# Optimization experiments

Measured on AMD Instinct MI355X. Metric: run time of the kernel, lower is better.

Reference implementation:

```python
import jax, jax.numpy as jnp
import numpy as np

B = 2
N_PER = 100000
M_PER = 27648
C = 32
Z, Y, X = 21, 400, 352
MAX_RANGE = (2, 2, 2)
RADIUS = 8.0
NSAMPLE = 16
VS = np.array([0.2, 0.2, 0.4], np.float32)  # voxel size (x, y, z)


def setup_inputs() -> dict:
    key = jax.random.key(0)
    ks = jax.random.split(key, 6)
    N = B * N_PER
    M = B * M_PER
    space = jnp.array([X * VS[0], Y * VS[1], Z * VS[2]], jnp.float32)
    xyz = jax.random.uniform(ks[0], (N, 3), jnp.float32) * space
    zc = jax.random.randint(ks[1], (M,), 0, Z)
    yc = jax.random.randint(ks[2], (M,), 0, Y)
    xc = jax.random.randint(ks[3], (M,), 0, X)
    bq = jnp.repeat(jnp.arange(B, dtype=jnp.int32), M_PER)
    new_coords = jnp.stack([bq, zc, yc, xc], 1).astype(jnp.int32)
    new_xyz = jnp.stack([(xc + 0.5) * VS[0], (yc + 0.5) * VS[1], (zc + 0.5) * VS[2]], 1).astype(jnp.float32)
    features = jax.random.normal(ks[4], (N, C), jnp.float32)
    raw = jax.random.randint(ks[5], (B, Z, Y, X), -N_PER, N_PER)
    offs = (jnp.arange(B) * N_PER)[:, None, None, None]
    voxel2point_indices = jnp.where(raw < 0, -1, raw + offs).astype(jnp.int32)
    xyz_batch_cnt = jnp.full((B,), N_PER, jnp.int32)
    new_xyz_batch_cnt = jnp.full((B,), M_PER, jnp.int32)
    return dict(new_coords=new_coords, xyz=xyz, xyz_batch_cnt=xyz_batch_cnt,
                new_xyz=new_xyz, new_xyz_batch_cnt=new_xyz_batch_cnt,
                features=features, voxel2point_indices=voxel2point_indices)


def _voxel_query(xyz, new_xyz, new_coords, point_indices):
    """Vectorized equivalent of the CUDA voxel_query kernel.
    Returns (idx (M, nsample) int32 global point indices, empty_ball_mask (M,) bool)."""
    zr, yr, xr = MAX_RANGE
    _, Zg, Yg, Xg = point_indices.shape
    M = new_coords.shape[0]
    dz, dy, dx = jnp.meshgrid(jnp.arange(-zr, zr + 1), jnp.arange(-yr, yr + 1),
                              jnp.arange(-xr, xr + 1), indexing='ij')
    offs = jnp.stack([dz.ravel(), dy.ravel(), dx.ravel()], 1)  # (K,3) in CUDA loop order z,y,x
    nb = new_coords[:, None, 1:4] + offs[None]                 # (M,K,3) candidate voxels
    lim = jnp.array([Zg, Yg, Xg])
    inb = jnp.all((nb >= 0) & (nb < lim), -1)                  # (M,K) in-bounds
    nbc = jnp.clip(nb, 0, lim - 1)
    b = new_coords[:, 0]
    pidx = point_indices[b[:, None], nbc[..., 0], nbc[..., 1], nbc[..., 2]]  # (M,K)
    valid = inb & (pidx >= 0)
    pts = xyz[jnp.maximum(pidx, 0)]                            # (M,K,3)
    d2 = jnp.sum((pts - new_xyz[:, None, :]) ** 2, -1)
    valid = valid & (d2 < RADIUS * RADIUS)
    cnt = jnp.minimum(valid.sum(-1), NSAMPLE)                  # (M,)
    # assign each valid candidate its in-order slot; overflow/invalid go to dump column
    slot = jnp.cumsum(valid, -1) - 1
    slot = jnp.where(valid & (slot < NSAMPLE), slot, NSAMPLE)
    rows = jnp.arange(M)[:, None]
    idx = jnp.zeros((M, NSAMPLE + 1), jnp.int32).at[rows, slot].set(pidx)[:, :NSAMPLE]
    first = idx[:, 0]  # CUDA pre-fills all slots with first found index
    idx = jnp.where(jnp.arange(NSAMPLE)[None, :] < cnt[:, None], idx, first[:, None])
    empty = cnt == 0
    idx = jnp.where(empty[:, None], 0, idx)
    return idx, empty


def reference(new_coords, xyz, xyz_batch_cnt, new_xyz, new_xyz_batch_cnt, features, voxel2point_indices):
    idx, empty = _voxel_query(xyz, new_xyz, new_coords, voxel2point_indices)
    # global -> batch-relative (as in the torch loop), empty balls -> 0 of their batch
    xyz_offs = jnp.concatenate([jnp.zeros(1, jnp.int32), jnp.cumsum(xyz_batch_cnt)[:-1].astype(jnp.int32)])
    qb = new_coords[:, 0]
    idx_rel = jnp.where(empty[:, None], 0, idx - xyz_offs[qb][:, None])
    # grouping_operation (stack version): gather with batch offset added back
    gidx = idx_rel + xyz_offs[qb][:, None]                     # (M, nsample) global indices
    grouped_xyz = jnp.transpose(xyz[gidx], (0, 2, 1))          # (M, 3, nsample)
    grouped_features = jnp.transpose(features[gidx], (0, 2, 1))  # (M, C, nsample)
    return grouped_features, grouped_xyz, empty
```

## Files before the change

kernel.cpp:

```cpp
#include <hip/hip_runtime.h>


constexpr int ZG = 21;
constexpr int YG = 400;
constexpr int XG = 352;
constexpr int NS = 16;
constexpr int CF = 32;
constexpr float R2 = 64.0f;

__global__ __launch_bounds__(256) void vqg_kernel(
    const int*   __restrict__ new_coords,
    const float* __restrict__ xyz,
    const int*   __restrict__ xyz_batch_cnt,
    const float* __restrict__ new_xyz,
    const float* __restrict__ features,
    const int*   __restrict__ v2p,
    float* __restrict__ out_feat,
    float* __restrict__ out_xyz,
    float* __restrict__ out_empty,
    int M)
{
    const int lane = threadIdx.x & 63;
    const int wid  = threadIdx.x >> 6;
    const int m    = blockIdx.x * 4 + wid;
    __shared__ int sg[4][NS];

    const bool active = (m < M);
    int cnt  = 0;
    int boff = 0;

    if (active) {
        const int4 qc = *reinterpret_cast<const int4*>(new_coords + (size_t)m * 4);
        const int b = qc.x, zc = qc.y, yc = qc.z, xc = qc.w;
        const float qx = new_xyz[m * 3 + 0];
        const float qy = new_xyz[m * 3 + 1];
        const float qz = new_xyz[m * 3 + 2];
        for (int i = 0; i < b; ++i) boff += xyz_batch_cnt[i];
        const int* __restrict__ gb = v2p + (size_t)b * (ZG * YG * XG);

        #pragma unroll
        for (int pass = 0; pass < 2; ++pass) {
            const int n = pass * 64 + lane;
            int  pidx  = -1;
            bool valid = false;
            if (n < 125) {
                const int dz = n / 25 - 2;
                const int dy = (n / 5) % 5 - 2;
                const int dx = n % 5 - 2;
                const int z = zc + dz, y = yc + dy, x = xc + dx;
                if ((unsigned)z < (unsigned)ZG && (unsigned)y < (unsigned)YG &&
                    (unsigned)x < (unsigned)XG) {
                    pidx = gb[((size_t)z * YG + y) * XG + x];
                    if (pidx >= 0) {
                        const float ddx = xyz[(size_t)pidx * 3 + 0] - qx;
                        const float ddy = xyz[(size_t)pidx * 3 + 1] - qy;
                        const float ddz = xyz[(size_t)pidx * 3 + 2] - qz;
                        const float d2 = __fadd_rn(
                            __fadd_rn(__fmul_rn(ddx, ddx), __fmul_rn(ddy, ddy)),
                            __fmul_rn(ddz, ddz));
                        valid = d2 < R2;
                    }
                }
            }
            const unsigned long long bal = __ballot(valid);
            const int pos = cnt + (int)__popcll(bal & ((1ull << lane) - 1ull));
            if (valid && pos < NS) sg[wid][pos] = pidx;
            cnt += (int)__popcll(bal);
            if (cnt >= NS) break;
        }
    }
    __syncthreads();

    if (active && lane < NS) {
        int g;
        if (cnt == 0) {
            g = boff;
        } else {
            const int first = sg[wid][0];
            const int c = cnt < NS ? cnt : NS;
            g = (lane < c) ? sg[wid][lane] : first;
        }
        sg[wid][lane] = g;
    }
    __syncthreads();

    if (active) {
        if (lane < 48) {
            const int s = lane & 15;
            const int d = lane >> 4;
            out_xyz[(size_t)m * 48 + d * 16 + s] =
                xyz[(size_t)sg[wid][s] * 3 + d];
        }
        if (lane == 0) out_empty[m] = (cnt == 0) ? 1.0f : 0.0f;

        float* __restrict__ of = out_feat + (size_t)m * (CF * NS);
        #pragma unroll
        for (int k = 0; k < 2; ++k) {
            const int f0 = k * 256 + lane * 4;
            const int c  = f0 >> 4;
            const int s0 = f0 & 15;
            float4 v;
            v.x = features[(size_t)sg[wid][s0 + 0] * CF + c];
            v.y = features[(size_t)sg[wid][s0 + 1] * CF + c];
            v.z = features[(size_t)sg[wid][s0 + 2] * CF + c];
            v.w = features[(size_t)sg[wid][s0 + 3] * CF + c];
            *reinterpret_cast<float4*>(of + f0) = v;
        }
    }
}

extern "C" void kernel_launch(void* const* d_in, const int* in_sizes, int n_in,
                              void* d_out, int out_size, void* d_ws, size_t ws_size,
                              hipStream_t stream) {
    const int*   new_coords    = (const int*)d_in[0];
    const float* xyz           = (const float*)d_in[1];
    const int*   xyz_batch_cnt = (const int*)d_in[2];
    const float* new_xyz       = (const float*)d_in[3];
    const float* features      = (const float*)d_in[5];
    const int*   v2p           = (const int*)d_in[6];

    const int M = in_sizes[0] / 4;

    float* out_feat  = (float*)d_out;
    float* out_xyz   = out_feat + (size_t)M * CF * NS;
    float* out_empty = out_xyz + (size_t)M * 3 * NS;

    const int blocks = (M + 3) / 4;
    vqg_kernel<<<blocks, 256, 0, stream>>>(
        new_coords, xyz, xyz_batch_cnt, new_xyz, features, v2p,
        out_feat, out_xyz, out_empty, M);
}
```

Baseline: 60.09 us.

## Stage features in LDS, pad xyz to float4, issue both neighbor passes together

Adds a prepass kernel that pads xyz into a float4 workspace copy, so each point load is a single 16-byte read. Both 64-lane neighbor passes now issue their voxel and point loads together instead of looping with an early break. Feature rows for the selected samples are read coalesced into a shared-memory tile, then transposed out with nontemporal float4 stores. In exchange it adds a second launch and a full pass over xyz, more shared memory per block, and an extra barrier. Early termination after 16 hits is gone.

```diff
diff --git a/kernel.cpp b/kernel.cpp
--- a/kernel.cpp
+++ b/kernel.cpp
@@ -8,13 +8,27 @@
 constexpr int CF = 32;
 constexpr float R2 = 64.0f;
 
+typedef float v4f __attribute__((ext_vector_type(4)));
+
+__global__ __launch_bounds__(256) void pad_xyz_kernel(
+    const float* __restrict__ xyz, float4* __restrict__ xyz4, int N)
+{
+    const int i = blockIdx.x * 256 + threadIdx.x;
+    if (i < N) {
+        const float* p = xyz + (size_t)i * 3;
+        xyz4[i] = make_float4(p[0], p[1], p[2], 0.0f);
+    }
+}
+
+template<bool USE4>
 __global__ __launch_bounds__(256) void vqg_kernel(
-    const int*   __restrict__ new_coords,
-    const float* __restrict__ xyz,
-    const int*   __restrict__ xyz_batch_cnt,
-    const float* __restrict__ new_xyz,
-    const float* __restrict__ features,
-    const int*   __restrict__ v2p,
+    const int*    __restrict__ new_coords,
+    const float*  __restrict__ xyz,
+    const float4* __restrict__ xyz4,
+    const int*    __restrict__ xyz_batch_cnt,
+    const float*  __restrict__ new_xyz,
+    const float*  __restrict__ features,
+    const int*    __restrict__ v2p,
     float* __restrict__ out_feat,
     float* __restrict__ out_xyz,
     float* __restrict__ out_empty,
@@ -23,7 +37,8 @@
     const int lane = threadIdx.x & 63;
     const int wid  = threadIdx.x >> 6;
     const int m    = blockIdx.x * 4 + wid;
-    __shared__ int sg[4][NS];
+    __shared__ int   sg[4][NS];
+    __shared__ float tile[4][NS][33];
 
     const bool active = (m < M);
     int cnt  = 0;
@@ -38,36 +53,71 @@
         for (int i = 0; i < b; ++i) boff += xyz_batch_cnt[i];
         const int* __restrict__ gb = v2p + (size_t)b * (ZG * YG * XG);
 
-        #pragma unroll
-        for (int pass = 0; pass < 2; ++pass) {
-            const int n = pass * 64 + lane;
-            int  pidx  = -1;
-            bool valid = false;
-            if (n < 125) {
-                const int dz = n / 25 - 2;
-                const int dy = (n / 5) % 5 - 2;
-                const int dx = n % 5 - 2;
-                const int z = zc + dz, y = yc + dy, x = xc + dx;
-                if ((unsigned)z < (unsigned)ZG && (unsigned)y < (unsigned)YG &&
-                    (unsigned)x < (unsigned)XG) {
-                    pidx = gb[((size_t)z * YG + y) * XG + x];
-                    if (pidx >= 0) {
-                        const float ddx = xyz[(size_t)pidx * 3 + 0] - qx;
-                        const float ddy = xyz[(size_t)pidx * 3 + 1] - qy;
-                        const float ddz = xyz[(size_t)pidx * 3 + 2] - qz;
-                        const float d2 = __fadd_rn(
-                            __fadd_rn(__fmul_rn(ddx, ddx), __fmul_rn(ddy, ddy)),
-                            __fmul_rn(ddz, ddz));
-                        valid = d2 < R2;
-                    }
-                }
+        const int n0 = lane;
+        const int n1 = 64 + lane;
+        int pidx0 = -1, pidx1 = -1;
+        {
+            const int z = zc + (n0 / 25 - 2);
+            const int y = yc + ((n0 / 5) % 5 - 2);
+            const int x = xc + (n0 % 5 - 2);
+            if ((unsigned)z < (unsigned)ZG && (unsigned)y < (unsigned)YG &&
+                (unsigned)x < (unsigned)XG)
+                pidx0 = gb[((size_t)z * YG + y) * XG + x];
+        }
+        if (n1 < 125) {
+            const int z = zc + (n1 / 25 - 2);
+            const int y = yc + ((n1 / 5) % 5 - 2);
+            const int x = xc + (n1 % 5 - 2);
+            if ((unsigned)z < (unsigned)ZG && (unsigned)y < (unsigned)YG &&
+                (unsigned)x < (unsigned)XG)
+                pidx1 = gb[((size_t)z * YG + y) * XG + x];
+        }
+
+        float p0x = 0, p0y = 0, p0z = 0, p1x = 0, p1y = 0, p1z = 0;
+        if (pidx0 >= 0) {
+            if (USE4) {
+                const float4 p = xyz4[pidx0];
+                p0x = p.x; p0y = p.y; p0z = p.z;
+            } else {
+                p0x = xyz[(size_t)pidx0 * 3 + 0];
+                p0y = xyz[(size_t)pidx0 * 3 + 1];
+                p0z = xyz[(size_t)pidx0 * 3 + 2];
             }
-            const unsigned long long bal = __ballot(valid);
-            const int pos = cnt + (int)__popcll(bal & ((1ull << lane) - 1ull));
-            if (valid && pos < NS) sg[wid][pos] = pidx;
-            cnt += (int)__popcll(bal);
-            if (cnt >= NS) break;
-        }
+        }
+        if (pidx1 >= 0) {
+            if (USE4) {
+                const float4 p = xyz4[pidx1];
+                p1x = p.x; p1y = p.y; p1z = p.z;
+            } else {
+                p1x = xyz[(size_t)pidx1 * 3 + 0];
+                p1y = xyz[(size_t)pidx1 * 3 + 1];
+                p1z = xyz[(size_t)pidx1 * 3 + 2];
+            }
+        }
+
+        bool v0 = false, v1 = false;
+        if (pidx0 >= 0) {
+            const float dx = p0x - qx, dy = p0y - qy, dz = p0z - qz;
+            const float d2 = __fadd_rn(__fadd_rn(__fmul_rn(dx, dx), __fmul_rn(dy, dy)),
+                                       __fmul_rn(dz, dz));
+            v0 = d2 < R2;
+        }
+        if (pidx1 >= 0) {
+            const float dx = p1x - qx, dy = p1y - qy, dz = p1z - qz;
+            const float d2 = __fadd_rn(__fadd_rn(__fmul_rn(dx, dx), __fmul_rn(dy, dy)),
+                                       __fmul_rn(dz, dz));
+            v1 = d2 < R2;
+        }
+
+        const unsigned long long below = (1ull << lane) - 1ull;
+        const unsigned long long bal0 = __ballot(v0);
+        const unsigned long long bal1 = __ballot(v1);
+        const int c0   = (int)__popcll(bal0);
+        const int pos0 = (int)__popcll(bal0 & below);
+        const int pos1 = c0 + (int)__popcll(bal1 & below);
+        if (v0 && pos0 < NS) sg[wid][pos0] = pidx0;
+        if (v1 && pos1 < NS) sg[wid][pos1] = pidx1;
+        cnt = c0 + (int)__popcll(bal1);
     }
     __syncthreads();
 
@@ -76,11 +126,20 @@
         if (cnt == 0) {
             g = boff;
         } else {
-            const int first = sg[wid][0];
             const int c = cnt < NS ? cnt : NS;
-            g = (lane < c) ? sg[wid][lane] : first;
+            g = (lane < c) ? sg[wid][lane] : sg[wid][0];
         }
         sg[wid][lane] = g;
+    }
+    __syncthreads();
+
+    const int K = active ? (cnt > 0 ? (cnt < NS ? cnt : NS) : 1) : 0;
+    if (active) {
+        const int half = lane >> 5;
+        const int c    = lane & 31;
+        for (int r = half; r < K; r += 2) {
+            tile[wid][r][c] = features[(size_t)sg[wid][r] * CF + c];
+        }
     }
     __syncthreads();
 
@@ -88,23 +147,27 @@
         if (lane < 48) {
             const int s = lane & 15;
             const int d = lane >> 4;
-            out_xyz[(size_t)m * 48 + d * 16 + s] =
-                xyz[(size_t)sg[wid][s] * 3 + d];
-        }
-        if (lane == 0) out_empty[m] = (cnt == 0) ? 1.0f : 0.0f;
+            const int row = sg[wid][s];
+            const float val = USE4 ? reinterpret_cast<const float*>(xyz4 + row)[d]
+                                   : xyz[(size_t)row * 3 + d];
+            __builtin_nontemporal_store(val, out_xyz + (size_t)m * 48 + d * 16 + s);
+        }
+        if (lane == 0)
+            __builtin_nontemporal_store(cnt == 0 ? 1.0f : 0.0f, out_empty + m);
 
         float* __restrict__ of = out_feat + (size_t)m * (CF * NS);
         #pragma unroll
         for (int k = 0; k < 2; ++k) {
-            const int f0 = k * 256 + lane * 4;
-            const int c  = f0 >> 4;
-            const int s0 = f0 & 15;
-            float4 v;
-            v.x = features[(size_t)sg[wid][s0 + 0] * CF + c];
-            v.y = features[(size_t)sg[wid][s0 + 1] * CF + c];
-            v.z = features[(size_t)sg[wid][s0 + 2] * CF + c];
-            v.w = features[(size_t)sg[wid][s0 + 3] * CF + c];
-            *reinterpret_cast<float4*>(of + f0) = v;
+            const int c  = k * 16 + (lane >> 2);
+            const int s0 = (lane & 3) * 4;
+            v4f v;
+            #pragma unroll
+            for (int j = 0; j < 4; ++j) {
+                const int s = s0 + j;
+                v[j] = tile[wid][s < K ? s : 0][c];
+            }
+            __builtin_nontemporal_store(
+                v, reinterpret_cast<v4f*>(of + k * 256 + (lane << 2)));
         }
     }
 }
@@ -120,13 +183,24 @@
     const int*   v2p           = (const int*)d_in[6];
 
     const int M = in_sizes[0] / 4;
+    const int N = in_sizes[1] / 3;
 
     float* out_feat  = (float*)d_out;
     float* out_xyz   = out_feat + (size_t)M * CF * NS;
     float* out_empty = out_xyz + (size_t)M * 3 * NS;
 
     const int blocks = (M + 3) / 4;
-    vqg_kernel<<<blocks, 256, 0, stream>>>(
-        new_coords, xyz, xyz_batch_cnt, new_xyz, features, v2p,
-        out_feat, out_xyz, out_empty, M);
+    const bool use4 = ws_size >= (size_t)N * sizeof(float4);
+
+    if (use4) {
+        float4* xyz4 = (float4*)d_ws;
+        pad_xyz_kernel<<<(N + 255) / 256, 256, 0, stream>>>(xyz, xyz4, N);
+        vqg_kernel<true><<<blocks, 256, 0, stream>>>(
+            new_coords, xyz, xyz4, xyz_batch_cnt, new_xyz, features, v2p,
+            out_feat, out_xyz, out_empty, M);
+    } else {
+        vqg_kernel<false><<<blocks, 256, 0, stream>>>(
+            new_coords, xyz, nullptr, xyz_batch_cnt, new_xyz, features, v2p,
+            out_feat, out_xyz, out_empty, M);
+    }
 }
```

Result: slower. 61.85 us (+2.9%).

## Process two queries per wavefront with register permutes instead of shared memory

Applied to the files above, without the earlier changes.

Each wavefront now handles two queries and issues all four voxel-grid lookups and their xyz loads up front, so the memory requests overlap instead of running in dependent passes. Compaction of valid neighbour indices moves from shared memory with __syncthreads to ds_permute and shuffles, and the outputs are written with nontemporal stores. It also drops the early exit once 16 neighbours are found, so the second-pass loads are always issued, and it raises register pressure.

```diff
diff --git a/kernel.cpp b/kernel.cpp
--- a/kernel.cpp
+++ b/kernel.cpp
@@ -7,6 +7,14 @@
 constexpr int NS = 16;
 constexpr int CF = 32;
 constexpr float R2 = 64.0f;
+
+typedef float v4f __attribute__((ext_vector_type(4)));
+
+struct QState {
+    int  cnt;
+    int  boff;
+    int  gfin;
+};
 
 __global__ __launch_bounds__(256) void vqg_kernel(
     const int*   __restrict__ new_coords,
@@ -21,90 +29,170 @@
     int M)
 {
     const int lane = threadIdx.x & 63;
-    const int wid  = threadIdx.x >> 6;
-    const int m    = blockIdx.x * 4 + wid;
-    __shared__ int sg[4][NS];
-
-    const bool active = (m < M);
-    int cnt  = 0;
-    int boff = 0;
-
-    if (active) {
-        const int4 qc = *reinterpret_cast<const int4*>(new_coords + (size_t)m * 4);
-        const int b = qc.x, zc = qc.y, yc = qc.z, xc = qc.w;
-        const float qx = new_xyz[m * 3 + 0];
-        const float qy = new_xyz[m * 3 + 1];
-        const float qz = new_xyz[m * 3 + 2];
-        for (int i = 0; i < b; ++i) boff += xyz_batch_cnt[i];
-        const int* __restrict__ gb = v2p + (size_t)b * (ZG * YG * XG);
-
-        #pragma unroll
-        for (int pass = 0; pass < 2; ++pass) {
-            const int n = pass * 64 + lane;
-            int  pidx  = -1;
-            bool valid = false;
-            if (n < 125) {
-                const int dz = n / 25 - 2;
-                const int dy = (n / 5) % 5 - 2;
-                const int dx = n % 5 - 2;
-                const int z = zc + dz, y = yc + dy, x = xc + dx;
-                if ((unsigned)z < (unsigned)ZG && (unsigned)y < (unsigned)YG &&
-                    (unsigned)x < (unsigned)XG) {
-                    pidx = gb[((size_t)z * YG + y) * XG + x];
-                    if (pidx >= 0) {
-                        const float ddx = xyz[(size_t)pidx * 3 + 0] - qx;
-                        const float ddy = xyz[(size_t)pidx * 3 + 1] - qy;
-                        const float ddz = xyz[(size_t)pidx * 3 + 2] - qz;
-                        const float d2 = __fadd_rn(
-                            __fadd_rn(__fmul_rn(ddx, ddx), __fmul_rn(ddy, ddy)),
-                            __fmul_rn(ddz, ddz));
-                        valid = d2 < R2;
-                    }
-                }
+    const int w    = (blockIdx.x * 256 + threadIdx.x) >> 6;
+    const int m0   = w * 2;
+    const int m1   = m0 + 1;
+    if (m0 >= M) return;
+    const bool has1 = (m1 < M);
+
+    const int4 qc0 = *reinterpret_cast<const int4*>(new_coords + (size_t)m0 * 4);
+    const int4 qc1 = has1 ? *reinterpret_cast<const int4*>(new_coords + (size_t)m1 * 4) : qc0;
+    const float qx0 = new_xyz[m0 * 3 + 0], qy0 = new_xyz[m0 * 3 + 1], qz0 = new_xyz[m0 * 3 + 2];
+    const float qx1 = has1 ? new_xyz[m1 * 3 + 0] : 0.f;
+    const float qy1 = has1 ? new_xyz[m1 * 3 + 1] : 0.f;
+    const float qz1 = has1 ? new_xyz[m1 * 3 + 2] : 0.f;
+
+    int boff0 = 0, boff1 = 0;
+    for (int i = 0; i < qc0.x; ++i) boff0 += xyz_batch_cnt[i];
+    for (int i = 0; i < qc1.x; ++i) boff1 += xyz_batch_cnt[i];
+
+    const int n0 = lane;
+    const int n1 = 64 + lane;
+    const int dz0 = n0 / 25 - 2, dy0 = (n0 / 5) % 5 - 2, dx0 = n0 % 5 - 2;
+    const int dz1 = n1 / 25 - 2, dy1 = (n1 / 5) % 5 - 2, dx1 = n1 % 5 - 2;
+    const bool in1 = (n1 < 125);
+
+    const int* __restrict__ gb0 = v2p + (size_t)qc0.x * (ZG * YG * XG);
+    const int* __restrict__ gb1 = v2p + (size_t)qc1.x * (ZG * YG * XG);
+
+    int pa0 = -1, pa1 = -1, pb0 = -1, pb1 = -1;
+    {
+        const int z = qc0.y + dz0, y = qc0.z + dy0, x = qc0.w + dx0;
+        if ((unsigned)z < (unsigned)ZG && (unsigned)y < (unsigned)YG && (unsigned)x < (unsigned)XG)
+            pa0 = gb0[((size_t)z * YG + y) * XG + x];
+    }
+    {
+        const int z = qc0.y + dz1, y = qc0.z + dy1, x = qc0.w + dx1;
+        if (in1 && (unsigned)z < (unsigned)ZG && (unsigned)y < (unsigned)YG && (unsigned)x < (unsigned)XG)
+            pa1 = gb0[((size_t)z * YG + y) * XG + x];
+    }
+    if (has1) {
+        const int z = qc1.y + dz0, y = qc1.z + dy0, x = qc1.w + dx0;
+        if ((unsigned)z < (unsigned)ZG && (unsigned)y < (unsigned)YG && (unsigned)x < (unsigned)XG)
+            pb0 = gb1[((size_t)z * YG + y) * XG + x];
+    }
+    if (has1) {
+        const int z = qc1.y + dz1, y = qc1.z + dy1, x = qc1.w + dx1;
+        if (in1 && (unsigned)z < (unsigned)ZG && (unsigned)y < (unsigned)YG && (unsigned)x < (unsigned)XG)
+            pb1 = gb1[((size_t)z * YG + y) * XG + x];
+    }
+
+    float a0x = 0, a0y = 0, a0z = 0, a1x = 0, a1y = 0, a1z = 0;
+    float b0x = 0, b0y = 0, b0z = 0, b1x = 0, b1y = 0, b1z = 0;
+    if (pa0 >= 0) { const float* p = xyz + (size_t)pa0 * 3; a0x = p[0]; a0y = p[1]; a0z = p[2]; }
+    if (pa1 >= 0) { const float* p = xyz + (size_t)pa1 * 3; a1x = p[0]; a1y = p[1]; a1z = p[2]; }
+    if (pb0 >= 0) { const float* p = xyz + (size_t)pb0 * 3; b0x = p[0]; b0y = p[1]; b0z = p[2]; }
+    if (pb1 >= 0) { const float* p = xyz + (size_t)pb1 * 3; b1x = p[0]; b1y = p[1]; b1z = p[2]; }
+
+    bool va0 = false, va1 = false, vb0 = false, vb1 = false;
+    if (pa0 >= 0) {
+        const float dx = a0x - qx0, dy = a0y - qy0, dz = a0z - qz0;
+        va0 = __fadd_rn(__fadd_rn(__fmul_rn(dx, dx), __fmul_rn(dy, dy)), __fmul_rn(dz, dz)) < R2;
+    }
+    if (pa1 >= 0) {
+        const float dx = a1x - qx0, dy = a1y - qy0, dz = a1z - qz0;
+        va1 = __fadd_rn(__fadd_rn(__fmul_rn(dx, dx), __fmul_rn(dy, dy)), __fmul_rn(dz, dz)) < R2;
+    }
+    if (pb0 >= 0) {
+        const float dx = b0x - qx1, dy = b0y - qy1, dz = b0z - qz1;
+        vb0 = __fadd_rn(__fadd_rn(__fmul_rn(dx, dx), __fmul_rn(dy, dy)), __fmul_rn(dz, dz)) < R2;
+    }
+    if (pb1 >= 0) {
+        const float dx = b1x - qx1, dy = b1y - qy1, dz = b1z - qz1;
+        vb1 = __fadd_rn(__fadd_rn(__fmul_rn(dx, dx), __fmul_rn(dy, dy)), __fmul_rn(dz, dz)) < R2;
+    }
+
+    const unsigned long long below = (1ull << lane) - 1ull;
+    const int junk = (16 + (lane & 31)) << 2;
+
+    int cnt0, gfin0;
+    {
+        const unsigned long long bal0 = __ballot(va0);
+        const unsigned long long bal1 = __ballot(va1);
+        const int c0   = (int)__popcll(bal0);
+        cnt0 = c0 + (int)__popcll(bal1);
+        const int pos0 = (int)__popcll(bal0 & below);
+        const int pos1 = c0 + (int)__popcll(bal1 & below);
+        const int addr0 = (va0 && pos0 < NS) ? (pos0 << 2) : junk;
+        const int addr1 = (va1 && pos1 < NS) ? (pos1 << 2) : junk;
+        const int perm0 = __builtin_amdgcn_ds_permute(addr0, pa0);
+        const int perm1 = __builtin_amdgcn_ds_permute(addr1, pa1);
+        const int sel   = (lane < c0) ? perm0 : perm1;
+        const int first = __shfl(sel, 0);
+        const int c16   = cnt0 < NS ? cnt0 : NS;
+        gfin0 = (cnt0 == 0) ? boff0 : (((lane & 15) < c16) ? sel : first);
+    }
+    int cnt1 = 0, gfin1 = 0;
+    if (has1) {
+        const unsigned long long bal0 = __ballot(vb0);
+        const unsigned long long bal1 = __ballot(vb1);
+        const int c0   = (int)__popcll(bal0);
+        cnt1 = c0 + (int)__popcll(bal1);
+        const int pos0 = (int)__popcll(bal0 & below);
+        const int pos1 = c0 + (int)__popcll(bal1 & below);
+        const int addr0 = (vb0 && pos0 < NS) ? (pos0 << 2) : junk;
+        const int addr1 = (vb1 && pos1 < NS) ? (pos1 << 2) : junk;
+        const int perm0 = __builtin_amdgcn_ds_permute(addr0, pb0);
+        const int perm1 = __builtin_amdgcn_ds_permute(addr1, pb1);
+        const int sel   = (lane < c0) ? perm0 : perm1;
+        const int first = __shfl(sel, 0);
+        const int c16   = cnt1 < NS ? cnt1 : NS;
+        gfin1 = (cnt1 == 0) ? boff1 : (((lane & 15) < c16) ? sel : first);
+    }
+
+    const int s0lane = (lane & 3) << 2;
+    const int a_r0 = __shfl(gfin0, s0lane + 0);
+    const int a_r1 = __shfl(gfin0, s0lane + 1);
+    const int a_r2 = __shfl(gfin0, s0lane + 2);
+    const int a_r3 = __shfl(gfin0, s0lane + 3);
+    const int b_r0 = __shfl(gfin1, s0lane + 0);
+    const int b_r1 = __shfl(gfin1, s0lane + 1);
+    const int b_r2 = __shfl(gfin1, s0lane + 2);
+    const int b_r3 = __shfl(gfin1, s0lane + 3);
+
+    {
+        const int s = lane & 15;
+        const int d = lane >> 4;
+        if (lane < 48) {
+            const int row = __shfl(gfin0, s);
+            __builtin_nontemporal_store(xyz[(size_t)row * 3 + d],
+                                        out_xyz + (size_t)m0 * 48 + d * 16 + s);
+        }
+        if (lane == 0)
+            __builtin_nontemporal_store(cnt0 == 0 ? 1.0f : 0.0f, out_empty + m0);
+        if (has1) {
+            if (lane < 48) {
+                const int row = __shfl(gfin1, s);
+                __builtin_nontemporal_store(xyz[(size_t)row * 3 + d],
+                                            out_xyz + (size_t)m1 * 48 + d * 16 + s);
             }
-            const unsigned long long bal = __ballot(valid);
-            const int pos = cnt + (int)__popcll(bal & ((1ull << lane) - 1ull));
-            if (valid && pos < NS) sg[wid][pos] = pidx;
-            cnt += (int)__popcll(bal);
-            if (cnt >= NS) break;
+            if (lane == 0)
+                __builtin_nontemporal_store(cnt1 == 0 ? 1.0f : 0.0f, out_empty + m1);
         }
     }
-    __syncthreads();
-
-    if (active && lane < NS) {
-        int g;
-        if (cnt == 0) {
-            g = boff;
-        } else {
-            const int first = sg[wid][0];
-            const int c = cnt < NS ? cnt : NS;
-            g = (lane < c) ? sg[wid][lane] : first;
-        }
-        sg[wid][lane] = g;
-    }
-    __syncthreads();
-
-    if (active) {
-        if (lane < 48) {
-            const int s = lane & 15;
-            const int d = lane >> 4;
-            out_xyz[(size_t)m * 48 + d * 16 + s] =
-                xyz[(size_t)sg[wid][s] * 3 + d];
-        }
-        if (lane == 0) out_empty[m] = (cnt == 0) ? 1.0f : 0.0f;
-
-        float* __restrict__ of = out_feat + (size_t)m * (CF * NS);
+
+    float* __restrict__ of0 = out_feat + (size_t)m0 * (CF * NS);
+    float* __restrict__ of1 = out_feat + (size_t)m1 * (CF * NS);
+    #pragma unroll
+    for (int k = 0; k < 2; ++k) {
+        const int c = k * 16 + (lane >> 2);
+        v4f v;
+        v[0] = features[(size_t)a_r0 * CF + c];
+        v[1] = features[(size_t)a_r1 * CF + c];
+        v[2] = features[(size_t)a_r2 * CF + c];
+        v[3] = features[(size_t)a_r3 * CF + c];
+        __builtin_nontemporal_store(v, reinterpret_cast<v4f*>(of0 + k * 256 + (lane << 2)));
+    }
+    if (has1) {
         #pragma unroll
         for (int k = 0; k < 2; ++k) {
-            const int f0 = k * 256 + lane * 4;
-            const int c  = f0 >> 4;
-            const int s0 = f0 & 15;
-            float4 v;
-            v.x = features[(size_t)sg[wid][s0 + 0] * CF + c];
-            v.y = features[(size_t)sg[wid][s0 + 1] * CF + c];
-            v.z = features[(size_t)sg[wid][s0 + 2] * CF + c];
-            v.w = features[(size_t)sg[wid][s0 + 3] * CF + c];
-            *reinterpret_cast<float4*>(of + f0) = v;
+            const int c = k * 16 + (lane >> 2);
+            v4f v;
+            v[0] = features[(size_t)b_r0 * CF + c];
+            v[1] = features[(size_t)b_r1 * CF + c];
+            v[2] = features[(size_t)b_r2 * CF + c];
+            v[3] = features[(size_t)b_r3 * CF + c];
+            __builtin_nontemporal_store(v, reinterpret_cast<v4f*>(of1 + k * 256 + (lane << 2)));
         }
     }
 }
@@ -125,7 +213,8 @@
     float* out_xyz   = out_feat + (size_t)M * CF * NS;
     float* out_empty = out_xyz + (size_t)M * 3 * NS;
 
-    const int blocks = (M + 3) / 4;
+    const int waves  = (M + 1) / 2;
+    const int blocks = (waves + 3) / 4;
     vqg_kernel<<<blocks, 256, 0, stream>>>(
         new_coords, xyz, xyz_batch_cnt, new_xyz, features, v2p,
         out_feat, out_xyz, out_empty, M);
```

Result: faster. 53.43 us (-11.1%).

## Process four queries per wavefront with register-only compaction and batched loads

Applied to the files above, without the earlier changes.

Each wavefront now handles four queries instead of one. All grid lookups, point-coordinate loads and feature gathers for those queries are issued up front to increase memory-level parallelism. Shared memory and __syncthreads are replaced by ballot plus ds_permute compaction and shuffles, and outputs use nontemporal stores. In exchange there are four times fewer wavefronts, higher register pressure, and the early exit once sixteen neighbours are found is gone, so the second pass is always loaded.

```diff
diff --git a/kernel.cpp b/kernel.cpp
--- a/kernel.cpp
+++ b/kernel.cpp
@@ -7,6 +7,9 @@
 constexpr int NS = 16;
 constexpr int CF = 32;
 constexpr float R2 = 64.0f;
+constexpr int QPW = 4;
+
+typedef float v4f __attribute__((ext_vector_type(4)));
 
 __global__ __launch_bounds__(256) void vqg_kernel(
     const int*   __restrict__ new_coords,
@@ -21,90 +24,153 @@
     int M)
 {
     const int lane = threadIdx.x & 63;
-    const int wid  = threadIdx.x >> 6;
-    const int m    = blockIdx.x * 4 + wid;
-    __shared__ int sg[4][NS];
+    const int w    = (blockIdx.x * 256 + threadIdx.x) >> 6;
+    const int mb   = w * QPW;
+    if (mb >= M) return;
 
-    const bool active = (m < M);
-    int cnt  = 0;
-    int boff = 0;
+    bool has[QPW];
+    #pragma unroll
+    for (int q = 0; q < QPW; ++q) has[q] = (mb + q) < M;
 
-    if (active) {
-        const int4 qc = *reinterpret_cast<const int4*>(new_coords + (size_t)m * 4);
-        const int b = qc.x, zc = qc.y, yc = qc.z, xc = qc.w;
-        const float qx = new_xyz[m * 3 + 0];
-        const float qy = new_xyz[m * 3 + 1];
-        const float qz = new_xyz[m * 3 + 2];
-        for (int i = 0; i < b; ++i) boff += xyz_batch_cnt[i];
-        const int* __restrict__ gb = v2p + (size_t)b * (ZG * YG * XG);
+    int4  qc[QPW];
+    float qx[QPW], qy[QPW], qz[QPW];
+    int   boff[QPW];
+    #pragma unroll
+    for (int q = 0; q < QPW; ++q) {
+        const int m = has[q] ? (mb + q) : mb;
+        qc[q] = *reinterpret_cast<const int4*>(new_coords + (size_t)m * 4);
+        qx[q] = new_xyz[m * 3 + 0];
+        qy[q] = new_xyz[m * 3 + 1];
+        qz[q] = new_xyz[m * 3 + 2];
+        int bo = 0;
+        for (int i = 0; i < qc[q].x; ++i) bo += xyz_batch_cnt[i];
+        boff[q] = bo;
+    }
 
-        #pragma unroll
-        for (int pass = 0; pass < 2; ++pass) {
-            const int n = pass * 64 + lane;
-            int  pidx  = -1;
-            bool valid = false;
-            if (n < 125) {
-                const int dz = n / 25 - 2;
-                const int dy = (n / 5) % 5 - 2;
-                const int dx = n % 5 - 2;
-                const int z = zc + dz, y = yc + dy, x = xc + dx;
-                if ((unsigned)z < (unsigned)ZG && (unsigned)y < (unsigned)YG &&
-                    (unsigned)x < (unsigned)XG) {
-                    pidx = gb[((size_t)z * YG + y) * XG + x];
-                    if (pidx >= 0) {
-                        const float ddx = xyz[(size_t)pidx * 3 + 0] - qx;
-                        const float ddy = xyz[(size_t)pidx * 3 + 1] - qy;
-                        const float ddz = xyz[(size_t)pidx * 3 + 2] - qz;
-                        const float d2 = __fadd_rn(
-                            __fadd_rn(__fmul_rn(ddx, ddx), __fmul_rn(ddy, ddy)),
-                            __fmul_rn(ddz, ddz));
-                        valid = d2 < R2;
-                    }
-                }
-            }
-            const unsigned long long bal = __ballot(valid);
-            const int pos = cnt + (int)__popcll(bal & ((1ull << lane) - 1ull));
-            if (valid && pos < NS) sg[wid][pos] = pidx;
-            cnt += (int)__popcll(bal);
-            if (cnt >= NS) break;
+    const int n1 = 64 + lane;
+    const int dz0 = lane / 25 - 2, dy0 = (lane / 5) % 5 - 2, dx0 = lane % 5 - 2;
+    const int dz1 = n1 / 25 - 2,   dy1 = (n1 / 5) % 5 - 2,   dx1 = n1 % 5 - 2;
+    const bool in1 = (n1 < 125);
+
+    int pidx[QPW][2];
+    #pragma unroll
+    for (int q = 0; q < QPW; ++q) {
+        const int* __restrict__ gb = v2p + (size_t)qc[q].x * (ZG * YG * XG);
+        pidx[q][0] = -1;
+        pidx[q][1] = -1;
+        {
+            const int z = qc[q].y + dz0, y = qc[q].z + dy0, x = qc[q].w + dx0;
+            if ((unsigned)z < (unsigned)ZG && (unsigned)y < (unsigned)YG &&
+                (unsigned)x < (unsigned)XG)
+                pidx[q][0] = gb[((size_t)z * YG + y) * XG + x];
+        }
+        {
+            const int z = qc[q].y + dz1, y = qc[q].z + dy1, x = qc[q].w + dx1;
+            if (in1 && (unsigned)z < (unsigned)ZG && (unsigned)y < (unsigned)YG &&
+                (unsigned)x < (unsigned)XG)
+                pidx[q][1] = gb[((size_t)z * YG + y) * XG + x];
         }
     }
-    __syncthreads();
 
-    if (active && lane < NS) {
-        int g;
-        if (cnt == 0) {
-            g = boff;
-        } else {
-            const int first = sg[wid][0];
-            const int c = cnt < NS ? cnt : NS;
-            g = (lane < c) ? sg[wid][lane] : first;
+    float px[QPW][2], py[QPW][2], pz[QPW][2];
+    #pragma unroll
+    for (int q = 0; q < QPW; ++q) {
+        #pragma unroll
+        for (int p = 0; p < 2; ++p) {
+            px[q][p] = 0.f; py[q][p] = 0.f; pz[q][p] = 0.f;
+            if (pidx[q][p] >= 0) {
+                const float* r = xyz + (size_t)pidx[q][p] * 3;
+                px[q][p] = r[0]; py[q][p] = r[1]; pz[q][p] = r[2];
+            }
         }
-        sg[wid][lane] = g;
     }
-    __syncthreads();
 
-    if (active) {
-        if (lane < 48) {
-            const int s = lane & 15;
-            const int d = lane >> 4;
-            out_xyz[(size_t)m * 48 + d * 16 + s] =
-                xyz[(size_t)sg[wid][s] * 3 + d];
+    bool val[QPW][2];
+    #pragma unroll
+    for (int q = 0; q < QPW; ++q) {
+        #pragma unroll
+        for (int p = 0; p < 2; ++p) {
+            bool v = false;
+            if (pidx[q][p] >= 0) {
+                const float dx = px[q][p] - qx[q];
+                const float dy = py[q][p] - qy[q];
+                const float dz = pz[q][p] - qz[q];
+                v = __fadd_rn(__fadd_rn(__fmul_rn(dx, dx), __fmul_rn(dy, dy)),
+                              __fmul_rn(dz, dz)) < R2;
+            }
+            val[q][p] = v;
         }
-        if (lane == 0) out_empty[m] = (cnt == 0) ? 1.0f : 0.0f;
+    }
 
-        float* __restrict__ of = out_feat + (size_t)m * (CF * NS);
+    const unsigned long long below = (1ull << lane) - 1ull;
+    const int junk = (16 + (lane & 31)) << 2;
+
+    int cnt[QPW], gfin[QPW];
+    #pragma unroll
+    for (int q = 0; q < QPW; ++q) {
+        const unsigned long long bal0 = __ballot(val[q][0]);
+        const unsigned long long bal1 = __ballot(val[q][1]);
+        const int c0   = (int)__popcll(bal0);
+        cnt[q] = c0 + (int)__popcll(bal1);
+        const int pos0 = (int)__popcll(bal0 & below);
+        const int pos1 = c0 + (int)__popcll(bal1 & below);
+        const int addr0 = (val[q][0] && pos0 < NS) ? (pos0 << 2) : junk;
+        const int addr1 = (val[q][1] && pos1 < NS) ? (pos1 << 2) : junk;
+        const int perm0 = __builtin_amdgcn_ds_permute(addr0, pidx[q][0]);
+        const int perm1 = __builtin_amdgcn_ds_permute(addr1, pidx[q][1]);
+        const int sel   = (lane < c0) ? perm0 : perm1;
+        const int first = __shfl(sel, 0);
+        const int c16   = cnt[q] < NS ? cnt[q] : NS;
+        gfin[q] = (cnt[q] == 0) ? boff[q] : (((lane & 15) < c16) ? sel : first);
+    }
+
+    {
+        const int s = lane & 15;
+        const int d = lane >> 4;
+        #pragma unroll
+        for (int q = 0; q < QPW; ++q) {
+            if (!has[q]) continue;
+            const int m = mb + q;
+            if (lane < 48) {
+                const int row = __shfl(gfin[q], s);
+                __builtin_nontemporal_store(xyz[(size_t)row * 3 + d],
+                                            out_xyz + (size_t)m * 48 + d * 16 + s);
+            }
+            if (lane == 0)
+                __builtin_nontemporal_store(cnt[q] == 0 ? 1.0f : 0.0f, out_empty + m);
+        }
+    }
+
+    const int s0 = (lane & 3) << 2;
+    const int cA = (lane >> 2);
+    int rr[QPW][4];
+    #pragma unroll
+    for (int q = 0; q < QPW; ++q) {
+        rr[q][0] = __shfl(gfin[q], s0 + 0);
+        rr[q][1] = __shfl(gfin[q], s0 + 1);
+        rr[q][2] = __shfl(gfin[q], s0 + 2);
+        rr[q][3] = __shfl(gfin[q], s0 + 3);
+    }
+    v4f vv[QPW][2];
+    #pragma unroll
+    for (int q = 0; q < QPW; ++q) {
         #pragma unroll
         for (int k = 0; k < 2; ++k) {
-            const int f0 = k * 256 + lane * 4;
-            const int c  = f0 >> 4;
-            const int s0 = f0 & 15;
-            float4 v;
-            v.x = features[(size_t)sg[wid][s0 + 0] * CF + c];
-            v.y = features[(size_t)sg[wid][s0 + 1] * CF + c];
-            v.z = features[(size_t)sg[wid][s0 + 2] * CF + c];
-            v.w = features[(size_t)sg[wid][s0 + 3] * CF + c];
-            *reinterpret_cast<float4*>(of + f0) = v;
+            const int c = k * 16 + cA;
+            vv[q][k][0] = features[(size_t)rr[q][0] * CF + c];
+            vv[q][k][1] = features[(size_t)rr[q][1] * CF + c];
+            vv[q][k][2] = features[(size_t)rr[q][2] * CF + c];
+            vv[q][k][3] = features[(size_t)rr[q][3] * CF + c];
+        }
+    }
+    #pragma unroll
+    for (int q = 0; q < QPW; ++q) {
+        if (!has[q]) continue;
+        float* __restrict__ of = out_feat + (size_t)(mb + q) * (CF * NS);
+        #pragma unroll
+        for (int k = 0; k < 2; ++k) {
+            __builtin_nontemporal_store(
+                vv[q][k], reinterpret_cast<v4f*>(of + k * 256 + (lane << 2)));
         }
     }
 }
@@ -125,7 +191,8 @@
     float* out_xyz   = out_feat + (size_t)M * CF * NS;
     float* out_empty = out_xyz + (size_t)M * 3 * NS;
 
-    const int blocks = (M + 3) / 4;
+    const int waves  = (M + QPW - 1) / QPW;
+    const int blocks = (waves + 3) / 4;
     vqg_kernel<<<blocks, 256, 0, stream>>>(
         new_coords, xyz, xyz_batch_cnt, new_xyz, features, v2p,
         out_feat, out_xyz, out_empty, M);
```

Result: faster. 56.59 us (-5.8%).
